# Kernel tuning notes

Hardware: AMD Instinct MI355X
Metric: run time of the kernel (lower is better)

Reference implementation:

```python
import jax, jax.numpy as jnp
import numpy as np

HEADS = 16  # config.heads


def setup_inputs() -> dict:
    key = jax.random.key(0)
    k1, k2, k3, k4 = jax.random.split(key, 4)
    B, S, H = 2, 2048, 2048
    x = jax.random.normal(k1, (B, S, H), dtype=jnp.float32)
    w_qkv = jax.random.normal(k2, (H, 3 * H), dtype=jnp.float32) * 0.02
    b_qkv = jax.random.normal(k3, (3 * H,), dtype=jnp.float32) * 0.02
    w_o = jax.random.normal(k4, (H, H), dtype=jnp.float32) * 0.02
    return {"x": x, "w_qkv": w_qkv, "b_qkv": b_qkv, "w_o": w_o}


def reference(x, w_qkv, b_qkv, w_o):
    # pre_layer_norm=False path: plain linear QKV projection
    B, S, H = x.shape
    hd = H // HEADS  # head_size
    scale = 1.0 / jnp.sqrt(jnp.float32(hd))  # 1/norm_factor^2, use_mup=False
    qkv = x @ w_qkv + b_qkv  # [B, S, 3H]
    q, k, v = qkv[..., :H], qkv[..., H:2 * H], qkv[..., 2 * H:]

    def split_heads(t):  # [B,S,H] -> [B,heads,S,hd]
        return t.reshape(B, S, HEADS, hd).transpose(0, 2, 1, 3)

    qh, kh, vh = split_heads(q), split_heads(k), split_heads(v)
    # score_4d_matmul with triangular masking + scale
    scores = jnp.einsum('bhqd,bhkd->bhqk', qh, kh) * scale  # [B,h,S,S]
    causal = jnp.tril(jnp.ones((S, S), dtype=bool))
    scores = jnp.where(causal, scores, -jnp.inf)
    probs = jax.nn.softmax(scores, axis=-1)
    # context_4d_matmul -> merge heads back to [B,S,H]
    ctx = jnp.einsum('bhqk,bhkd->bhqd', probs, vh)
    ctx = ctx.transpose(0, 2, 1, 3).reshape(B, S, H)
    # vector_matmul with attn_ow (no bias in this path)
    out = ctx @ w_o
    return out
```

## Files before the change

### kernel.cpp

```cpp
#include <hip/hip_runtime.h>
#include <cstdint>
#include <cstddef>

typedef __attribute__((ext_vector_type(8))) short bf16x8;
typedef __attribute__((ext_vector_type(4))) float f32x4;
typedef __attribute__((ext_vector_type(4))) unsigned short ushort4_;

#define MFMA16(a, b, c) __builtin_amdgcn_mfma_f32_16x16x32_bf16((a), (b), (c), 0, 0, 0)

__device__ __forceinline__ unsigned short f2bf(float f) {
  union { float f; unsigned u; } c; c.f = f;
  unsigned r = c.u + 0x7fffu + ((c.u >> 16) & 1u);
  return (unsigned short)(r >> 16);
}

__device__ __forceinline__ void gl_lds16(const unsigned short* g, unsigned short* l) {
  __builtin_amdgcn_global_load_lds(
      (const __attribute__((address_space(1))) void*)g,
      (__attribute__((address_space(3))) void*)l, 16, 0, 0);
}

__global__ __launch_bounds__(256) void k_prep(const float* __restrict__ x,
                                              unsigned short* __restrict__ xb,
                                              const float* __restrict__ wqkv,
                                              unsigned short* __restrict__ wqkvT,
                                              const float* __restrict__ wo,
                                              unsigned short* __restrict__ woT) {
  __shared__ unsigned short t[64][65];
  const int blk = blockIdx.x;
  const int tid = threadIdx.x;
  if (blk < 8192) {
    int i = blk * 256 + tid;
    float4 v = reinterpret_cast<const float4*>(x)[i];
    ushort4_ o;
    o.x = f2bf(v.x); o.y = f2bf(v.y); o.z = f2bf(v.z); o.w = f2bf(v.w);
    reinterpret_cast<ushort4_*>(xb)[i] = o;
    return;
  }
  const float* W;
  unsigned short* WT;
  int n0, k0, N;
  if (blk < 11264) {
    int local = blk - 8192;
    W = wqkv; WT = wqkvT; N = 6144;
    n0 = (local % 96) * 64; k0 = (local / 96) * 64;
  } else {
    int local = blk - 11264;
    W = wo; WT = woT; N = 2048;
    n0 = (local % 32) * 64; k0 = (local / 32) * 64;
  }
#pragma unroll
  for (int i = 0; i < 16; i++) {
    int li = tid + i * 256;
    int kk = li >> 6, nn = li & 63;
    t[kk][nn] = f2bf(W[(size_t)(k0 + kk) * N + (n0 + nn)]);
  }
  __syncthreads();
#pragma unroll
  for (int i = 0; i < 16; i++) {
    int li = tid + i * 256;
    int nn = li >> 6, kk = li & 63;
    WT[(size_t)(n0 + nn) * 2048 + (k0 + kk)] = t[kk][nn];
  }
}

template <int MODE>
__global__ __launch_bounds__(256) void k_gemm(const unsigned short* __restrict__ A,
                                              const unsigned short* __restrict__ Bt,
                                              const float* __restrict__ bias,
                                              unsigned short* __restrict__ qb,
                                              unsigned short* __restrict__ kb,
                                              unsigned short* __restrict__ vtb,
                                              float* __restrict__ outp) {
  __shared__ __align__(16) unsigned short As[128 * 64];
  __shared__ __align__(16) unsigned short Bs[128 * 64];
  const int tid = threadIdx.x;
  const int lane = tid & 63, wid = tid >> 6;
  const int quad = lane >> 4, l16 = lane & 15;
  const int wm = wid >> 1, wn = wid & 1;
  const int m0 = blockIdx.y * 128, n0 = blockIdx.x * 128;

  f32x4 acc[4][4];
#pragma unroll
  for (int i = 0; i < 4; i++)
#pragma unroll
    for (int j = 0; j < 4; j++) {
      f32x4 z = {0.f, 0.f, 0.f, 0.f};
      acc[i][j] = z;
    }

  for (int k0 = 0; k0 < 2048; k0 += 64) {
    __syncthreads();
#pragma unroll
    for (int i = 0; i < 4; i++) {
      int slotbase = wid * 64 + i * 256;
      int slot = slotbase + lane;
      int row = slot >> 3, chs = slot & 7, gch = chs ^ (row & 7);
      gl_lds16(A + (size_t)(m0 + row) * 2048 + k0 + gch * 8, &As[slotbase * 8]);
      gl_lds16(Bt + (size_t)(n0 + row) * 2048 + k0 + gch * 8, &Bs[slotbase * 8]);
    }
    __syncthreads();
#pragma unroll
    for (int kc = 0; kc < 2; kc++) {
      bf16x8 af[4], bfr[4];
#pragma unroll
      for (int mt = 0; mt < 4; mt++) {
        int r = wm * 64 + mt * 16 + l16;
        int ch = kc * 4 + quad;
        af[mt] = *reinterpret_cast<const bf16x8*>(&As[r * 64 + ((ch ^ (r & 7)) * 8)]);
      }
#pragma unroll
      for (int nt = 0; nt < 4; nt++) {
        int r = wn * 64 + nt * 16 + l16;
        int ch = kc * 4 + quad;
        bfr[nt] = *reinterpret_cast<const bf16x8*>(&Bs[r * 64 + ((ch ^ (r & 7)) * 8)]);
      }
#pragma unroll
      for (int mt = 0; mt < 4; mt++)
#pragma unroll
        for (int nt = 0; nt < 4; nt++)
          acc[mt][nt] = MFMA16(af[mt], bfr[nt], acc[mt][nt]);
    }
  }

  const int mbase = m0 + wm * 64;
  const int nbase = n0 + wn * 64;
  if (MODE == 0) {
#pragma unroll
    for (int nt = 0; nt < 4; nt++) {
      int n = nbase + nt * 16 + l16;
      float bv = bias[n];
      int seg = n >> 11;
      int h = (n >> 7) & 15;
      int d = n & 127;
#pragma unroll
      for (int mt = 0; mt < 4; mt++) {
        int mrow = mbase + mt * 16 + quad * 4;
        int b = mrow >> 11, s = mrow & 2047;
        if (seg == 2) {
          ushort4_ pk;
          pk.x = f2bf(acc[mt][nt][0] + bv);
          pk.y = f2bf(acc[mt][nt][1] + bv);
          pk.z = f2bf(acc[mt][nt][2] + bv);
          pk.w = f2bf(acc[mt][nt][3] + bv);
          *reinterpret_cast<ushort4_*>(vtb + ((size_t)(b * 16 + h) * 128 + d) * 2048 + s) = pk;
        } else {
          unsigned short* dst = (seg == 0 ? qb : kb);
          size_t base = (size_t)(b * 16 + h) * 2048;
#pragma unroll
          for (int rg = 0; rg < 4; rg++)
            dst[(base + (s + rg)) * 128 + d] = f2bf(acc[mt][nt][rg] + bv);
        }
      }
    }
  } else {
#pragma unroll
    for (int nt = 0; nt < 4; nt++) {
      int n = nbase + nt * 16 + l16;
#pragma unroll
      for (int mt = 0; mt < 4; mt++) {
        int mrow = mbase + mt * 16 + quad * 4;
#pragma unroll
        for (int rg = 0; rg < 4; rg++)
          outp[(size_t)(mrow + rg) * 2048 + n] = acc[mt][nt][rg];
      }
    }
  }
}

__global__ __launch_bounds__(256, 2) void k_attn(const unsigned short* __restrict__ qb,
                                                 const unsigned short* __restrict__ kb,
                                                 const unsigned short* __restrict__ vtb,
                                                 unsigned short* __restrict__ ctx) {
  __shared__ __align__(16) unsigned short Ks[2][64 * 128];
  __shared__ __align__(16) unsigned short Vs[2][128 * 64];
  __shared__ __align__(16) unsigned short Ps[128 * 64];
  const int bx = blockIdx.x;
  const int g = (bx & 1) ? (15 - (bx >> 1)) : (bx >> 1);
  const int qt = (blockIdx.y < 16) ? g : (15 - g);
  const int bh = blockIdx.y;
  const int tid = threadIdx.x;
  const int lane = tid & 63, w = tid >> 6;
  const int quad = lane >> 4, l16 = lane & 15;
  const int qbase = qt * 128;
  const unsigned short* Qh = qb + (size_t)bh * 2048 * 128;
  const unsigned short* Kh = kb + (size_t)bh * 2048 * 128;
  const unsigned short* Vh = vtb + (size_t)bh * 128 * 2048;

  const int q_lo = qbase + w * 32;
  const int nkv = 2 * qt + 2;
  const float sl2 = 0.12751741f;

  bf16x8 qf[2][4];
#pragma unroll
  for (int half = 0; half < 2; half++)
#pragma unroll
    for (int kc = 0; kc < 4; kc++)
      qf[half][kc] = *reinterpret_cast<const bf16x8*>(
          Qh + (size_t)(q_lo + half * 16 + l16) * 128 + kc * 32 + quad * 8);

  f32x4 o[2][8];
#pragma unroll
  for (int half = 0; half < 2; half++)
#pragma unroll
    for (int dt = 0; dt < 8; dt++) {
      f32x4 z = {0.f, 0.f, 0.f, 0.f};
      o[half][dt] = z;
    }
  float m_run[2] = {-1e30f, -1e30f}, l_run[2] = {0.f, 0.f};

  auto stage = [&](int kvb, int bsel) {
    unsigned short* Kd = &Ks[bsel][0];
    unsigned short* Vd = &Vs[bsel][0];
#pragma unroll
    for (int i = 0; i < 4; i++) {
      int slotbase = i * 256 + w * 64;
      int slot = slotbase + lane;
      int rowk = slot >> 4, chk = (slot & 15) ^ (rowk & 7);
      gl_lds16(Kh + (size_t)(kvb + rowk) * 128 + chk * 8, Kd + slotbase * 8);
      int rowv = slot >> 3, chv = (slot & 7) ^ (rowv & 7);
      gl_lds16(Vh + (size_t)rowv * 2048 + kvb + chv * 8, Vd + slotbase * 8);
    }
  };

  stage(0, 0);

  for (int kv = 0; kv < nkv; kv++) {
    const int kvb = kv * 64;
    const int cur = kv & 1;
    asm volatile("s_waitcnt vmcnt(0)" ::: "memory");
    asm volatile("s_barrier" ::: "memory");
    if (kv + 1 < nkv) stage(kvb + 64, cur ^ 1);
    if (kvb > q_lo + 31) continue;

    const unsigned short* Kc = &Ks[cur][0];
    const unsigned short* Vc = &Vs[cur][0];

    f32x4 sacc[2][4];
#pragma unroll
    for (int half = 0; half < 2; half++)
#pragma unroll
      for (int nt = 0; nt < 4; nt++) {
        f32x4 z = {0.f, 0.f, 0.f, 0.f};
        sacc[half][nt] = z;
      }
#pragma unroll
    for (int kc = 0; kc < 4; kc++) {
#pragma unroll
      for (int nt = 0; nt < 4; nt++) {
        int r = nt * 16 + l16, ch = kc * 4 + quad;
        bf16x8 kf = *reinterpret_cast<const bf16x8*>(&Kc[r * 128 + ((ch ^ (r & 7)) * 8)]);
        sacc[0][nt] = MFMA16(kf, qf[0][kc], sacc[0][nt]);
        sacc[1][nt] = MFMA16(kf, qf[1][kc], sacc[1][nt]);
      }
    }

    const bool needmask = (kvb + 63) > q_lo;
#pragma unroll
    for (int half = 0; half < 2; half++) {
      const int qabs = q_lo + half * 16 + l16;
      float tmax = -1e30f;
#pragma unroll
      for (int nt = 0; nt < 4; nt++)
#pragma unroll
        for (int rg = 0; rg < 4; rg++) {
          float v = sacc[half][nt][rg] * sl2;
          if (needmask && (kvb + nt * 16 + quad * 4 + rg) > qabs) v = -1e30f;
          sacc[half][nt][rg] = v;
          tmax = fmaxf(tmax, v);
        }
      tmax = fmaxf(tmax, __shfl_xor(tmax, 16));
      tmax = fmaxf(tmax, __shfl_xor(tmax, 32));
      float mnew = fmaxf(m_run[half], tmax);
      float alpha = exp2f(m_run[half] - mnew);
      m_run[half] = mnew;
      float rsum = 0.f;
#pragma unroll
      for (int nt = 0; nt < 4; nt++)
#pragma unroll
        for (int rg = 0; rg < 4; rg++) {
          float p = exp2f(sacc[half][nt][rg] - mnew);
          sacc[half][nt][rg] = p;
          rsum += p;
        }
      rsum += __shfl_xor(rsum, 16);
      rsum += __shfl_xor(rsum, 32);
      l_run[half] = l_run[half] * alpha + rsum;
#pragma unroll
      for (int dt = 0; dt < 8; dt++)
#pragma unroll
        for (int rg = 0; rg < 4; rg++) o[half][dt][rg] *= alpha;

#pragma unroll
      for (int nt = 0; nt < 4; nt++) {
        ushort4_ pk;
        pk.x = f2bf(sacc[half][nt][0]);
        pk.y = f2bf(sacc[half][nt][1]);
        pk.z = f2bf(sacc[half][nt][2]);
        pk.w = f2bf(sacc[half][nt][3]);
        int chunk = nt * 2 + (quad >> 1);
        *reinterpret_cast<ushort4_*>(
            &Ps[(w * 32 + half * 16 + l16) * 64 + ((chunk ^ (l16 & 7)) * 8) +
                (quad & 1) * 4]) = pk;
      }
    }
    asm volatile("s_waitcnt lgkmcnt(0)" ::: "memory");

#pragma unroll
    for (int kc = 0; kc < 2; kc++) {
      int chunkr = kc * 4 + quad;
      bf16x8 pf0 = *reinterpret_cast<const bf16x8*>(
          &Ps[(w * 32 + l16) * 64 + ((chunkr ^ (l16 & 7)) * 8)]);
      bf16x8 pf1 = *reinterpret_cast<const bf16x8*>(
          &Ps[(w * 32 + 16 + l16) * 64 + ((chunkr ^ (l16 & 7)) * 8)]);
#pragma unroll
      for (int dt = 0; dt < 8; dt++) {
        int r = dt * 16 + l16, ch = kc * 4 + quad;
        bf16x8 vf = *reinterpret_cast<const bf16x8*>(&Vc[r * 64 + ((ch ^ (r & 7)) * 8)]);
        o[0][dt] = MFMA16(vf, pf0, o[0][dt]);
        o[1][dt] = MFMA16(vf, pf1, o[1][dt]);
      }
    }
  }

  const int b = bh >> 4, h = bh & 15;
#pragma unroll
  for (int half = 0; half < 2; half++) {
    const float inv = 1.f / l_run[half];
    const int s = q_lo + half * 16 + l16;
#pragma unroll
    for (int dt = 0; dt < 8; dt++) {
      int d0 = dt * 16 + quad * 4;
      ushort4_ pk;
      pk.x = f2bf(o[half][dt][0] * inv);
      pk.y = f2bf(o[half][dt][1] * inv);
      pk.z = f2bf(o[half][dt][2] * inv);
      pk.w = f2bf(o[half][dt][3] * inv);
      *reinterpret_cast<ushort4_*>(
          &ctx[((size_t)b * 2048 + s) * 2048 + h * 128 + d0]) = pk;
    }
  }
}

extern "C" void kernel_launch(void* const* d_in, const int* in_sizes, int n_in,
                              void* d_out, int out_size, void* d_ws, size_t ws_size,
                              hipStream_t stream) {
  const float* x = (const float*)d_in[0];
  const float* w_qkv = (const float*)d_in[1];
  const float* b_qkv = (const float*)d_in[2];
  const float* w_o = (const float*)d_in[3];
  float* outp = (float*)d_out;

  unsigned short* ws = (unsigned short*)d_ws;
  unsigned short* xb    = ws;
  unsigned short* wqkvT = xb + 8388608;
  unsigned short* woT   = wqkvT + 12582912;
  unsigned short* qbuf  = woT + 4194304;
  unsigned short* kbuf  = qbuf + 8388608;
  unsigned short* vtbuf = kbuf + 8388608;
  unsigned short* ctxb  = vtbuf + 8388608;

  k_prep<<<12288, 256, 0, stream>>>(x, xb, w_qkv, wqkvT, w_o, woT);
  k_gemm<0><<<dim3(48, 32), 256, 0, stream>>>(xb, wqkvT, b_qkv, qbuf, kbuf, vtbuf, nullptr);
  k_attn<<<dim3(16, 32), 256, 0, stream>>>(qbuf, kbuf, vtbuf, ctxb);
  k_gemm<1><<<dim3(16, 32), 256, 0, stream>>>(ctxb, woT, nullptr, nullptr, nullptr, nullptr, outp);
}
```

Measured before the change: 392.5 us.

## Split QKV GEMM into three launches, lazy softmax rescale, MFMA priority hints

The fused QKV projection GEMM is split into three separate launches, one each for Q, K and V, so the epilogue branch on segment becomes a compile-time mode. In the attention kernel the running max and output rescale are skipped unless some row's max grows by more than a threshold of 8 (log2 units), which avoids the per-tile multiply of the output accumulators. s_setprio is raised around the MFMA loops. The split adds launch overhead and gives each launch a smaller grid of 512 blocks. The lazy rescale lets exponentials reach up to 2^8 before rescaling, which slightly reduces the numerical margin.

```diff
diff --git a/kernel.cpp b/kernel.cpp
--- a/kernel.cpp
+++ b/kernel.cpp
@@ -68,9 +68,7 @@
 __global__ __launch_bounds__(256) void k_gemm(const unsigned short* __restrict__ A,
                                               const unsigned short* __restrict__ Bt,
                                               const float* __restrict__ bias,
-                                              unsigned short* __restrict__ qb,
-                                              unsigned short* __restrict__ kb,
-                                              unsigned short* __restrict__ vtb,
+                                              unsigned short* __restrict__ dst,
                                               float* __restrict__ outp) {
   __shared__ __align__(16) unsigned short As[128 * 64];
   __shared__ __align__(16) unsigned short Bs[128 * 64];
@@ -125,44 +123,41 @@
 
   const int mbase = m0 + wm * 64;
   const int nbase = n0 + wn * 64;
-  if (MODE == 0) {
+  if (MODE == 3) {
+#pragma unroll
+    for (int nt = 0; nt < 4; nt++) {
+      int n = nbase + nt * 16 + l16;
+#pragma unroll
+      for (int mt = 0; mt < 4; mt++) {
+        int mrow = mbase + mt * 16 + quad * 4;
+#pragma unroll
+        for (int rg = 0; rg < 4; rg++)
+          outp[(size_t)(mrow + rg) * 2048 + n] = acc[mt][nt][rg];
+      }
+    }
+  } else {
 #pragma unroll
     for (int nt = 0; nt < 4; nt++) {
       int n = nbase + nt * 16 + l16;
       float bv = bias[n];
-      int seg = n >> 11;
-      int h = (n >> 7) & 15;
-      int d = n & 127;
+      int h = n >> 7, d = n & 127;
 #pragma unroll
       for (int mt = 0; mt < 4; mt++) {
         int mrow = mbase + mt * 16 + quad * 4;
         int b = mrow >> 11, s = mrow & 2047;
-        if (seg == 2) {
+        if (MODE == 2) {
           ushort4_ pk;
           pk.x = f2bf(acc[mt][nt][0] + bv);
           pk.y = f2bf(acc[mt][nt][1] + bv);
           pk.z = f2bf(acc[mt][nt][2] + bv);
           pk.w = f2bf(acc[mt][nt][3] + bv);
-          *reinterpret_cast<ushort4_*>(vtb + ((size_t)(b * 16 + h) * 128 + d) * 2048 + s) = pk;
+          *reinterpret_cast<ushort4_*>(dst + ((size_t)(b * 16 + h) * 128 + d) * 2048 + s) = pk;
         } else {
-          unsigned short* dst = (seg == 0 ? qb : kb);
           size_t base = (size_t)(b * 16 + h) * 2048;
 #pragma unroll
           for (int rg = 0; rg < 4; rg++)
             dst[(base + (s + rg)) * 128 + d] = f2bf(acc[mt][nt][rg] + bv);
         }
-      }
-    }
-  } else {
-#pragma unroll
-    for (int nt = 0; nt < 4; nt++) {
-      int n = nbase + nt * 16 + l16;
-#pragma unroll
-      for (int mt = 0; mt < 4; mt++) {
-        int mrow = mbase + mt * 16 + quad * 4;
-#pragma unroll
-        for (int rg = 0; rg < 4; rg++)
-          outp[(size_t)(mrow + rg) * 2048 + n] = acc[mt][nt][rg];
       }
     }
   }
@@ -244,6 +239,7 @@
         f32x4 z = {0.f, 0.f, 0.f, 0.f};
         sacc[half][nt] = z;
       }
+    __builtin_amdgcn_s_setprio(1);
 #pragma unroll
     for (int kc = 0; kc < 4; kc++) {
 #pragma unroll
@@ -254,6 +250,7 @@
         sacc[1][nt] = MFMA16(kf, qf[1][kc], sacc[1][nt]);
       }
     }
+    __builtin_amdgcn_s_setprio(0);
 
     const bool needmask = (kvb + 63) > q_lo;
 #pragma unroll
@@ -271,25 +268,29 @@
         }
       tmax = fmaxf(tmax, __shfl_xor(tmax, 16));
       tmax = fmaxf(tmax, __shfl_xor(tmax, 32));
-      float mnew = fmaxf(m_run[half], tmax);
-      float alpha = exp2f(m_run[half] - mnew);
-      m_run[half] = mnew;
+      if (!__all(tmax - m_run[half] <= 8.f)) {
+        float mnew = fmaxf(m_run[half], tmax);
+        float alpha = exp2f(m_run[half] - mnew);
+        m_run[half] = mnew;
+        l_run[half] *= alpha;
+#pragma unroll
+        for (int dt = 0; dt < 8; dt++)
+#pragma unroll
+          for (int rg = 0; rg < 4; rg++) o[half][dt][rg] *= alpha;
+      }
+      const float mcur = m_run[half];
       float rsum = 0.f;
 #pragma unroll
       for (int nt = 0; nt < 4; nt++)
 #pragma unroll
         for (int rg = 0; rg < 4; rg++) {
-          float p = exp2f(sacc[half][nt][rg] - mnew);
+          float p = exp2f(sacc[half][nt][rg] - mcur);
           sacc[half][nt][rg] = p;
           rsum += p;
         }
       rsum += __shfl_xor(rsum, 16);
       rsum += __shfl_xor(rsum, 32);
-      l_run[half] = l_run[half] * alpha + rsum;
-#pragma unroll
-      for (int dt = 0; dt < 8; dt++)
-#pragma unroll
-        for (int rg = 0; rg < 4; rg++) o[half][dt][rg] *= alpha;
+      l_run[half] += rsum;
 
 #pragma unroll
       for (int nt = 0; nt < 4; nt++) {
@@ -306,6 +307,7 @@
     }
     asm volatile("s_waitcnt lgkmcnt(0)" ::: "memory");
 
+    __builtin_amdgcn_s_setprio(1);
 #pragma unroll
     for (int kc = 0; kc < 2; kc++) {
       int chunkr = kc * 4 + quad;
@@ -321,6 +323,7 @@
         o[1][dt] = MFMA16(vf, pf1, o[1][dt]);
       }
     }
+    __builtin_amdgcn_s_setprio(0);
   }
 
   const int b = bh >> 4, h = bh & 15;
@@ -361,7 +364,9 @@
   unsigned short* ctxb  = vtbuf + 8388608;
 
   k_prep<<<12288, 256, 0, stream>>>(x, xb, w_qkv, wqkvT, w_o, woT);
-  k_gemm<0><<<dim3(48, 32), 256, 0, stream>>>(xb, wqkvT, b_qkv, qbuf, kbuf, vtbuf, nullptr);
+  k_gemm<0><<<dim3(16, 32), 256, 0, stream>>>(xb, wqkvT, b_qkv, qbuf, nullptr);
+  k_gemm<1><<<dim3(16, 32), 256, 0, stream>>>(xb, wqkvT + (size_t)4194304, b_qkv + 2048, kbuf, nullptr);
+  k_gemm<2><<<dim3(16, 32), 256, 0, stream>>>(xb, wqkvT + (size_t)8388608, b_qkv + 4096, vtbuf, nullptr);
   k_attn<<<dim3(16, 32), 256, 0, stream>>>(qbuf, kbuf, vtbuf, ctxb);
-  k_gemm<1><<<dim3(16, 32), 256, 0, stream>>>(ctxb, woT, nullptr, nullptr, nullptr, nullptr, outp);
-}
+  k_gemm<3><<<dim3(16, 32), 256, 0, stream>>>(ctxb, woT, nullptr, nullptr, outp);
+}
```

After: 405.9 us. +3.4%, slower.
